# Kernel tuning notes

Measured on AMD Instinct MI355X. Metric: run time of the kernel, lower is better.

## Reference

```python
import jax, jax.numpy as jnp
import numpy as np
import math

B, S, DM = 32, 512, 1024   # batch (= groups*channels), seq_len, d_model
H, D, C = 16, 64, 8        # n_heads, d_kv, n_channels
NB, MD = 32, 128           # relative_attention_num_buckets, max_distance


def setup_inputs() -> dict:
    key = jax.random.key(0)
    ks = jax.random.split(key, 7)
    return {
        "hidden_states": jax.random.normal(ks[0], (B, S, DM), jnp.float32),
        "Wq": jax.random.normal(ks[1], (DM, H * D), jnp.float32) * 0.02,
        "Wk": jax.random.normal(ks[2], (DM, H * D), jnp.float32) * 0.02,
        "Wv": jax.random.normal(ks[3], (DM, H * D), jnp.float32) * 0.02,
        "Wo": jax.random.normal(ks[4], (H * D, DM), jnp.float32) * 0.02,
        "rel_emb": jax.random.normal(ks[5], (NB, H), jnp.float32) * 0.02,
        "beta": jax.random.normal(ks[6], (1, 1, H, 1, 1), jnp.float32) * 0.01,
    }


def _rel_bucket(relative_position, num_buckets=NB, max_distance=MD):
    # bidirectional (encoder) bucketing, faithful to T5
    nb = num_buckets // 2
    buckets = (relative_position > 0).astype(jnp.int32) * nb
    rp = jnp.abs(relative_position)
    max_exact = nb // 2
    is_small = rp < max_exact
    rp_safe = jnp.maximum(rp, 1).astype(jnp.float32)
    large = max_exact + (
        jnp.log(rp_safe / max_exact) / math.log(max_distance / max_exact) * (nb - max_exact)
    ).astype(jnp.int32)
    large = jnp.minimum(large, nb - 1)
    return buckets + jnp.where(is_small, rp, large)


def reference(hidden_states, Wq, Wk, Wv, Wo, rel_emb, beta):
    G = B // C  # groups

    def proj(W):
        # (B,S,DM) -> (B,S,H,D) -> (B,H,S,D) -> (G,C,H,S,D)
        x = (hidden_states @ W).reshape(B, S, H, D).transpose(0, 2, 1, 3)
        return x.reshape(G, C, H, S, D)

    q, k, v = proj(Wq), proj(Wk), proj(Wv)

    # relative position bias: (1,1,H,S,S)
    rel_pos = jnp.arange(S)[None, :] - jnp.arange(S)[:, None]
    bias = rel_emb[_rel_bucket(rel_pos)].transpose(2, 0, 1)[None, None]

    # local (dot-product) attention, T5-style: no 1/sqrt(d) scaling
    scores = jnp.einsum('gchsd,gchtd->gchst', q, k) + bias
    attn_w = jax.nn.softmax(scores, axis=-1)
    a_dot = jnp.einsum('gchst,gchtd->gchsd', attn_w, v)

    # compressive memory: ELU+1 feature map, summed over channels
    sk = jax.nn.elu(k) + 1.0
    M = jnp.einsum('gchsd,gchse->ghde', sk, v)   # (G,H,D,D)
    z = sk.sum(axis=3).sum(axis=1)               # (G,H,D)
    sq = jax.nn.elu(q) + 1.0
    num = jnp.einsum('gchsd,ghde->gchse', sq, M)
    den = jnp.einsum('gchsd,ghd->gchs', sq, z)[..., None] + 1e-6
    a_mem = num / den

    gate = jax.nn.sigmoid(beta)  # (1,1,H,1,1)
    out = gate * a_mem + (1.0 - gate) * a_dot

    # (G,C,H,S,D) -> (B,H,S,D) -> (B,S,H*D)
    out = out.reshape(B, H, S, D).transpose(0, 2, 1, 3).reshape(B, S, H * D)
    return out @ Wo
```

## Files before the change

kernel.cpp:

```cpp
#include <hip/hip_runtime.h>
#include <stdint.h>

typedef unsigned short u16;
typedef u16 u16x8 __attribute__((ext_vector_type(8)));
typedef u16 u16x4 __attribute__((ext_vector_type(4)));
typedef __bf16 bf16x8 __attribute__((ext_vector_type(8)));
typedef float f32x4 __attribute__((ext_vector_type(4)));

#define DEV static __device__ __forceinline__

DEV u16 f2bf(float f) {
  union { float f; uint32_t u; } v; v.f = f;
  uint32_t r = v.u + 0x7FFFu + ((v.u >> 16) & 1u);
  return (u16)(r >> 16);
}
DEV float bf2f(u16 s) {
  union { uint32_t u; float f; } v; v.u = ((uint32_t)s) << 16;
  return v.f;
}
DEV float elu1(float x) { return x > 0.f ? x + 1.f : __expf(x); }
DEV u16x8 ld8u(const u16* p) { return *reinterpret_cast<const u16x8*>(p); }

DEV f32x4 mfma16(u16x8 a, u16x8 b, f32x4 c) {
  return __builtin_amdgcn_mfma_f32_16x16x32_bf16(
      __builtin_bit_cast(bf16x8, a), __builtin_bit_cast(bf16x8, b), c, 0, 0, 0);
}
DEV void async16(void* lds, const void* g) {
  __builtin_amdgcn_global_load_lds(
      (__attribute__((address_space(1))) void*)g,
      (__attribute__((address_space(3))) void*)lds, 16, 0, 0);
}

#define BARR __builtin_amdgcn_s_barrier()
#define LG0  asm volatile("s_waitcnt lgkmcnt(0)" ::: "memory")
#define VMC(N) asm volatile("s_waitcnt vmcnt(" #N ")" ::: "memory")


__global__ __launch_bounds__(256) void k_cvt(const float* __restrict__ in, u16* __restrict__ out) {
  int i = blockIdx.x * 256 + threadIdx.x;
  const float4* p = reinterpret_cast<const float4*>(in) + (size_t)i * 2;
  float4 a = p[0], b = p[1];
  u16x8 o;
  o[0] = f2bf(a.x); o[1] = f2bf(a.y); o[2] = f2bf(a.z); o[3] = f2bf(a.w);
  o[4] = f2bf(b.x); o[5] = f2bf(b.y); o[6] = f2bf(b.z); o[7] = f2bf(b.w);
  reinterpret_cast<u16x8*>(out)[i] = o;
}

__global__ __launch_bounds__(1024) void k_tr(const float* __restrict__ Wq, const float* __restrict__ Wk,
                                             const float* __restrict__ Wv, const float* __restrict__ Wo,
                                             u16* __restrict__ wt, u16* __restrict__ wot) {
  __shared__ float tb[32][33];
  int mat = blockIdx.x >> 10;
  int tile = blockIdx.x & 1023;
  int n0 = (tile >> 5) * 32;
  int k0 = (tile & 31) * 32;
  const float* W = (mat == 0) ? Wq : (mat == 1) ? Wk : (mat == 2) ? Wv : Wo;
  int tx = threadIdx.x & 31, ty = threadIdx.x >> 5;
  tb[ty][tx] = W[(size_t)(k0 + ty) * 1024 + n0 + tx];
  __syncthreads();
  u16 v = f2bf(tb[tx][ty]);
  if (mat < 3) wt[(size_t)(mat * 1024 + n0 + ty) * 1024 + k0 + tx] = v;
  else         wot[(size_t)(n0 + ty) * 1024 + k0 + tx] = v;
}

__global__ void k_bias(const float* __restrict__ rel, float* __restrict__ bias) {
  int off = blockIdx.x * 256 + threadIdx.x;
  if (off >= 1023) return;
  int rp = off - 511;
  int bck = rp > 0 ? 16 : 0;
  int arp = rp < 0 ? -rp : rp;
  int idx;
  if (arp < 8) idx = arp;
  else {
    float l = logf((float)arp * 0.125f) / logf(16.0f) * 8.0f;
    int lg = 8 + (int)l;
    idx = lg < 15 ? lg : 15;
  }
  bck += idx;
  for (int h = 0; h < 16; ++h) bias[h * 1023 + off] = rel[bck * 16 + h];
}


template <int EPI>
__global__ __launch_bounds__(512, 3) void k_g256(const u16* __restrict__ A, const u16* __restrict__ Bt,
                                                 u16* __restrict__ oq, u16* __restrict__ ok2,
                                                 u16* __restrict__ ovt, float* __restrict__ of) {
  __shared__ __align__(16) u16 lsA[2][128 * 32];
  __shared__ __align__(16) u16 lsB[2][256 * 32];
  const int t = threadIdx.x;
  const int lane = t & 63, w = t >> 6;
  const int wm = w >> 2, wn = w & 3;
  const int lr = lane & 15, lg = lane >> 4;

  const int bid = blockIdx.x;
  const int xcd = bid & 7, local = bid >> 3;
  const int s = local >> 4, w16 = local & 15;
  const int msq = s & 3, nsq = s >> 2;
  const int m0 = (xcd * 16 + msq * 4 + (w16 >> 2)) * 128;
  const int n0 = (nsq * 4 + (w16 & 3)) * 256;

  auto stage = [&](int kt, int slot) {
    const int k0 = kt * 32;
    {
      int c = t, S = c >> 3, q = (c & 7) ^ (S & 7);
      int row = 2 * S + (q >> 2), u = q & 3;
      async16(&lsA[slot][c * 8], A + (size_t)(m0 + row) * 1024 + k0 + u * 8);
    }
#pragma unroll
    for (int i = 0; i < 2; ++i) {
      int c = i * 512 + t, S = c >> 3, q = (c & 7) ^ (S & 7);
      int row = 2 * S + (q >> 2), u = q & 3;
      async16(&lsB[slot][c * 8], Bt + (size_t)(n0 + row) * 1024 + k0 + u * 8);
    }
  };
  auto rdoff = [&](int r_) -> int {
    return (r_ >> 1) * 64 + (((((r_ & 1) << 2) + lg) ^ ((r_ >> 1) & 7)) << 3);
  };

  f32x4 acc[4][4];
#pragma unroll
  for (int i = 0; i < 4; ++i)
#pragma unroll
    for (int j = 0; j < 4; ++j) acc[i][j] = (f32x4){0.f, 0.f, 0.f, 0.f};

  stage(0, 0);
  stage(1, 1);
  VMC(3);
  BARR;

  for (int kt = 0; kt < 32; ++kt) {
    const int slot = kt & 1;
    const u16* la = &lsA[slot][0];
    const u16* lb = &lsB[slot][0];

    u16x8 af[4], bf[4];
#pragma unroll
    for (int mi = 0; mi < 4; ++mi) af[mi] = ld8u(la + rdoff(wm * 64 + mi * 16 + lr));
#pragma unroll
    for (int ni = 0; ni < 4; ++ni) bf[ni] = ld8u(lb + rdoff(wn * 64 + ni * 16 + lr));
    LG0;
    BARR;
    if (kt + 2 < 32) stage(kt + 2, slot);

    __builtin_amdgcn_s_setprio(1);
#pragma unroll
    for (int mi = 0; mi < 4; ++mi)
#pragma unroll
      for (int ni = 0; ni < 4; ++ni)
        acc[mi][ni] = mfma16(af[mi], bf[ni], acc[mi][ni]);
    __builtin_amdgcn_s_setprio(0);

    if (kt + 2 < 32)      { VMC(3); }
    else if (kt == 30)    { VMC(0); }
    BARR;
  }

  if (EPI == 0) {
    const int which = n0 >> 10;
    const int nb = (n0 & 1023) + wn * 64;
#pragma unroll
    for (int mi = 0; mi < 4; ++mi)
#pragma unroll
      for (int r = 0; r < 4; ++r) {
        int m = m0 + wm * 64 + mi * 16 + lg * 4 + r;
        int b = m >> 9, s2 = m & 511;
#pragma unroll
        for (int ni = 0; ni < 4; ++ni) {
          int nc = nb + ni * 16 + lr;
          int h = nc >> 6, d = nc & 63;
          int bh = b * 16 + h;
          u16 v = f2bf(acc[mi][ni][r]);
          if (which == 0)      oq[(size_t)(bh * 512 + s2) * 64 + d] = v;
          else if (which == 1) ok2[(size_t)(bh * 512 + s2) * 64 + d] = v;
          else                 ovt[(size_t)(bh * 64 + d) * 512 + s2] = v;
        }
      }
  } else {
#pragma unroll
    for (int mi = 0; mi < 4; ++mi)
#pragma unroll
      for (int r = 0; r < 4; ++r) {
        int m = m0 + wm * 64 + mi * 16 + lg * 4 + r;
#pragma unroll
        for (int ni = 0; ni < 4; ++ni) {
          int n = n0 + wn * 64 + ni * 16 + lr;
          of[(size_t)m * 1024 + n] = acc[mi][ni][r];
        }
      }
  }
}


__global__ __launch_bounds__(256) void k_mem(const u16* __restrict__ K, const u16* __restrict__ Vt,
                                             float* __restrict__ Mp, float* __restrict__ zp) {
  __shared__ __align__(16) u16 skT[64 * 128];
  __shared__ __align__(16) u16 lV[64 * 128];
  __shared__ float mbuf[64][65];
  __shared__ float zsh[4][64];
  const int bid = blockIdx.x;
  const int g = bid >> 7, h = (bid >> 3) & 15, c = bid & 7;
  const int bh = (g * 8 + c) * 16 + h;
  const u16* kp = K + (size_t)bh * 512 * 64;
  const u16* vp = Vt + (size_t)bh * 64 * 512;
  const int t = threadIdx.x, lane = t & 63, w = t >> 6;
  const int lr = lane & 15, lg = lane >> 4;
  const int dmy = t & 63, sq = t >> 6;

  f32x4 acc[4][4];
#pragma unroll
  for (int i = 0; i < 4; ++i)
#pragma unroll
    for (int j = 0; j < 4; ++j) acc[i][j] = (f32x4){0.f, 0.f, 0.f, 0.f};
  float zacc = 0.f;

  for (int s0 = 0; s0 < 512; s0 += 128) {
#pragma unroll
    for (int i = 0; i < 4; ++i) {
      int c2 = i * 256 + t;
      int row = c2 >> 4, u = c2 & 15;
      async16(lV + c2 * 8, vp + (size_t)row * 512 + s0 + ((u ^ (row & 7)) << 3));
    }
#pragma unroll
    for (int r = 0; r < 4; ++r) {
      const int un = sq + r * 4;
      const int ss0 = un * 8;
      u16x8 vals;
#pragma unroll
      for (int j = 0; j < 8; ++j) {
        float x = elu1(bf2f(kp[(size_t)(s0 + ss0 + j) * 64 + dmy]));
        zacc += x;
        vals[j] = f2bf(x);
      }
      *reinterpret_cast<u16x8*>(skT + dmy * 128 + ((un ^ (dmy & 7)) << 3)) = vals;
    }
    VMC(0);
    __syncthreads();
    u16x8 af[4], bfv[4];
#pragma unroll
    for (int ds = 0; ds < 4; ++ds) {
      const int d = ds * 16 + lr;
      af[ds] = ld8u(skT + d * 128 + (((w * 4 + lg) ^ (d & 7)) << 3));
    }
#pragma unroll
    for (int es = 0; es < 4; ++es) {
      const int e = es * 16 + lr;
      bfv[es] = ld8u(lV + e * 128 + (((w * 4 + lg) ^ (e & 7)) << 3));
    }
#pragma unroll
    for (int ds = 0; ds < 4; ++ds)
#pragma unroll
      for (int es = 0; es < 4; ++es) acc[ds][es] = mfma16(af[ds], bfv[es], acc[ds][es]);
    __syncthreads();
  }

  zsh[sq][dmy] = zacc;
  for (int wv = 0; wv < 4; ++wv) {
    if (w == wv) {
#pragma unroll
      for (int ds = 0; ds < 4; ++ds)
#pragma unroll
        for (int es = 0; es < 4; ++es)
#pragma unroll
          for (int r = 0; r < 4; ++r) {
            int d = ds * 16 + lg * 4 + r, e = es * 16 + lr;
            if (wv == 0) mbuf[d][e] = acc[ds][es][r];
            else         mbuf[d][e] += acc[ds][es][r];
          }
    }
    __syncthreads();
  }
#pragma unroll
  for (int j = 0; j < 16; ++j) {
    int idx = j * 256 + t;
    Mp[(size_t)bid * 4096 + idx] = mbuf[idx >> 6][idx & 63];
  }
  if (t < 64) zp[(size_t)bid * 64 + t] = zsh[0][t] + zsh[1][t] + zsh[2][t] + zsh[3][t];
}

__global__ __launch_bounds__(256) void k_red(const float* __restrict__ Mp, const float* __restrict__ zp,
                                             u16* __restrict__ Mt, float* __restrict__ zv) {
  const int gh = blockIdx.x;
  const int t = threadIdx.x;
#pragma unroll
  for (int j = 0; j < 16; ++j) {
    int idx = j * 256 + t;
    int d = idx >> 6, e = idx & 63;
    float s = 0.f;
#pragma unroll
    for (int c = 0; c < 8; ++c) s += Mp[(size_t)(gh * 8 + c) * 4096 + idx];
    Mt[(size_t)gh * 4096 + e * 64 + d] = f2bf(s);
  }
  if (t < 64) {
    float s = 0.f;
#pragma unroll
    for (int c = 0; c < 8; ++c) s += zp[(size_t)(gh * 8 + c) * 64 + t];
    zv[gh * 64 + t] = s;
  }
}


__global__ __launch_bounds__(256, 4) void k_attn(const u16* __restrict__ Q, const u16* __restrict__ K,
                                                 const u16* __restrict__ Vt, const u16* __restrict__ Mt,
                                                 const float* __restrict__ zv, const float* __restrict__ bias,
                                                 const float* __restrict__ beta, u16* __restrict__ blend) {
  __shared__ __align__(16) u16 lK[64 * 64];
  __shared__ __align__(16) u16 lV[64 * 64];
  __shared__ __align__(16) u16 ps[4][32 * 64];
  __shared__ float lbias[1023];
  __shared__ float zs[64];
  __shared__ float rsl[4][32];
  __shared__ float dnl[4][32];

  const int bid = blockIdx.x;
  const int bh = bid >> 2, qg = bid & 3;
  const int b = bh >> 4, h = bh & 15, g = b >> 3;
  const int gh = g * 16 + h;
  const int t = threadIdx.x, lane = t & 63, w = t >> 6;
  const int lr = lane & 15, lg = lane >> 4;
  const int q0w = qg * 128 + w * 32;
  const u16* qp = Q + (size_t)bh * 512 * 64;
  const u16* kp = K + (size_t)bh * 512 * 64;
  const u16* vp = Vt + (size_t)bh * 64 * 512;
  const u16* mp = Mt + (size_t)gh * 4096;
  const float gate = 1.f / (1.f + __expf(-beta[h]));
  u16* psw = &ps[w][0];

  for (int i = t; i < 1023; i += 256) lbias[i] = bias[h * 1023 + i];
  if (t < 64) zs[t] = zv[gh * 64 + t];

  u16x8 qf[2][2];
#pragma unroll
  for (int qs = 0; qs < 2; ++qs)
#pragma unroll
    for (int dc = 0; dc < 2; ++dc)
      qf[qs][dc] = ld8u(qp + (size_t)(q0w + qs * 16 + lr) * 64 + dc * 32 + lg * 8);

#pragma unroll
  for (int i = 0; i < 2; ++i) {
    int c = w * 128 + i * 64 + lane;
    int kr = c >> 3, u = c & 7;
    async16(lK + c * 8, kp + (size_t)kr * 64 + ((u ^ (kr & 7)) << 3));
    async16(lV + c * 8, vp + (size_t)kr * 512 + ((u ^ (kr & 7)) << 3));
  }
  __syncthreads();

#pragma unroll
  for (int qs = 0; qs < 2; ++qs) {
    float sum = 0.f;
#pragma unroll
    for (int dc = 0; dc < 2; ++dc)
#pragma unroll
      for (int j = 0; j < 8; ++j)
        sum += elu1(bf2f(qf[qs][dc][j])) * zs[dc * 32 + lg * 8 + j];
    sum += __shfl_xor(sum, 16, 64);
    sum += __shfl_xor(sum, 32, 64);
    if (lane < 16) dnl[w][qs * 16 + lane] = sum + 1e-6f;
  }

  f32x4 acc[2][4];
#pragma unroll
  for (int qs = 0; qs < 2; ++qs)
#pragma unroll
    for (int es = 0; es < 4; ++es) acc[qs][es] = (f32x4){0.f, 0.f, 0.f, 0.f};
  float rs[2] = {0.f, 0.f};

  for (int kt = 0; kt < 8; ++kt) {
#pragma unroll
    for (int ks = 0; ks < 4; ++ks) {
      const int kr = ks * 16 + lr;
      u16x8 kf0 = ld8u(lK + kr * 64 + (((0 * 4 + lg) ^ (kr & 7)) << 3));
      u16x8 kf1 = ld8u(lK + kr * 64 + (((1 * 4 + lg) ^ (kr & 7)) << 3));
#pragma unroll
      for (int qs = 0; qs < 2; ++qs) {
        f32x4 s = mfma16(kf0, qf[qs][0], (f32x4){0.f, 0.f, 0.f, 0.f});
        s = mfma16(kf1, qf[qs][1], s);
        const int bbase = kt * 64 + ks * 16 + lg * 4 - (q0w + qs * 16 + lr) + 511;
        u16x4 pk;
        float lsum = 0.f;
#pragma unroll
        for (int r = 0; r < 4; ++r) {
          float p = __expf(s[r] + lbias[bbase + r]);
          lsum += p;
          pk[r] = f2bf(p);
        }
        rs[qs] += lsum;
        const int row = qs * 16 + lr;
        const int addr = row * 64 + (((ks * 2 + (lg >> 1)) ^ (row & 7)) << 3) + (lg & 1) * 4;
        *reinterpret_cast<u16x4*>(psw + addr) = pk;
      }
    }
#pragma unroll
    for (int kc = 0; kc < 2; ++kc) {
      u16x8 pf[2];
#pragma unroll
      for (int qs = 0; qs < 2; ++qs) {
        const int row = qs * 16 + lr;
        pf[qs] = ld8u(psw + row * 64 + (((kc * 4 + lg) ^ (row & 7)) << 3));
      }
#pragma unroll
      for (int es = 0; es < 4; ++es) {
        const int er = es * 16 + lr;
        u16x8 vf = ld8u(lV + er * 64 + (((kc * 4 + lg) ^ (er & 7)) << 3));
#pragma unroll
        for (int qs = 0; qs < 2; ++qs) acc[qs][es] = mfma16(pf[qs], vf, acc[qs][es]);
      }
    }
    __syncthreads();
    if (kt + 1 < 8) {
#pragma unroll
      for (int i = 0; i < 2; ++i) {
        int c = w * 128 + i * 64 + lane;
        int kr = c >> 3, u = c & 7;
        async16(lK + c * 8, kp + (size_t)((kt + 1) * 64 + kr) * 64 + ((u ^ (kr & 7)) << 3));
        async16(lV + c * 8, vp + (size_t)kr * 512 + (kt + 1) * 64 + ((u ^ (kr & 7)) << 3));
      }
    }
    __syncthreads();
  }

#pragma unroll
  for (int qs = 0; qs < 2; ++qs) {
    float v = rs[qs];
    v += __shfl_xor(v, 16, 64);
    v += __shfl_xor(v, 32, 64);
    if (lane < 16) rsl[w][qs * 16 + lane] = 1.f / v;
  }

  u16x8 sqf[2][2];
#pragma unroll
  for (int qs = 0; qs < 2; ++qs)
#pragma unroll
    for (int dc = 0; dc < 2; ++dc)
#pragma unroll
      for (int j = 0; j < 8; ++j) sqf[qs][dc][j] = f2bf(elu1(bf2f(qf[qs][dc][j])));
  f32x4 am[2][4];
#pragma unroll
  for (int qs = 0; qs < 2; ++qs)
#pragma unroll
    for (int es = 0; es < 4; ++es) am[qs][es] = (f32x4){0.f, 0.f, 0.f, 0.f};
#pragma unroll
  for (int es = 0; es < 4; ++es)
#pragma unroll
    for (int dc = 0; dc < 2; ++dc) {
      u16x8 mf = ld8u(mp + (es * 16 + lr) * 64 + dc * 32 + lg * 8);
#pragma unroll
      for (int qs = 0; qs < 2; ++qs) am[qs][es] = mfma16(sqf[qs][dc], mf, am[qs][es]);
    }

#pragma unroll
  for (int qs = 0; qs < 2; ++qs)
#pragma unroll
    for (int r = 0; r < 4; ++r) {
      const int rowl = qs * 16 + lg * 4 + r;
      const float rinv = rsl[w][rowl];
      const float den = dnl[w][rowl];
      const int q = q0w + rowl;
#pragma unroll
      for (int es = 0; es < 4; ++es) {
        float o = gate * (am[qs][es][r] / den) + (1.f - gate) * acc[qs][es][r] * rinv;
        blend[(size_t)(b * 512 + q) * 1024 + h * 64 + es * 16 + lr] = f2bf(o);
      }
    }
}


extern "C" void kernel_launch(void* const* d_in, const int* in_sizes, int n_in,
                              void* d_out, int out_size, void* d_ws, size_t ws_size,
                              hipStream_t stream) {
  (void)in_sizes; (void)n_in; (void)out_size; (void)ws_size;
  const float* hs   = (const float*)d_in[0];
  const float* Wq   = (const float*)d_in[1];
  const float* Wk   = (const float*)d_in[2];
  const float* Wv   = (const float*)d_in[3];
  const float* Wo   = (const float*)d_in[4];
  const float* rel  = (const float*)d_in[5];
  const float* beta = (const float*)d_in[6];
  float* out = (float*)d_out;

  char* ws = (char*)d_ws;
  size_t off = 0;
  auto alloc = [&](size_t bytes) -> char* {
    char* p = ws + off;
    off += (bytes + 255) & ~(size_t)255;
    return p;
  };
  u16* hsb    = (u16*)alloc(16384ull * 1024 * 2);
  u16* wt     = (u16*)alloc(3072ull * 1024 * 2);
  u16* wot    = (u16*)alloc(1024ull * 1024 * 2);
  u16* q      = (u16*)alloc(16384ull * 1024 * 2);
  u16* k      = (u16*)alloc(16384ull * 1024 * 2);
  u16* vt     = (u16*)alloc(16384ull * 1024 * 2);
  float* Mp   = (float*)alloc(512ull * 4096 * 4);
  float* zp   = (float*)alloc(512ull * 64 * 4);
  u16* Mt     = (u16*)alloc(64ull * 4096 * 2);
  float* zv   = (float*)alloc(64ull * 64 * 4);
  float* bias = (float*)alloc(16ull * 1023 * 4);
  u16* blend  = hsb;

  k_cvt<<<8192, 256, 0, stream>>>(hs, hsb);
  k_tr<<<4096, 1024, 0, stream>>>(Wq, Wk, Wv, Wo, wt, wot);
  k_bias<<<4, 256, 0, stream>>>(rel, bias);
  k_g256<0><<<1536, 512, 0, stream>>>(hsb, wt, q, k, vt, nullptr);
  k_mem<<<512, 256, 0, stream>>>(k, vt, Mp, zp);
  k_red<<<64, 256, 0, stream>>>(Mp, zp, Mt, zv);
  k_attn<<<2048, 256, 0, stream>>>(q, k, vt, Mt, zv, bias, beta, blend);
  k_g256<1><<<512, 512, 0, stream>>>(blend, wot, nullptr, nullptr, nullptr, out);
}
```

Before: 341.7 us.

## Double-buffer K/V tiles in attention kernel and trim bias LDS window

Switches the attention kernel's K/V shared-memory tiles to two buffers, so the async load of the next tile is issued before computing on the current one, and waits with a partial vmcnt instead of a full sync-load-sync sequence. The relative-bias table in LDS is narrowed to the 640-entry window this query group needs, which offsets part of the extra LDS. Launch bounds drop from 4 to 3 blocks per CU to fit the larger shared footprint, which may reduce occupancy.

After: 339.4 us. Within noise of the previous version (-0.7%).

```diff
diff --git a/kernel.cpp b/kernel.cpp
--- a/kernel.cpp
+++ b/kernel.cpp
@@ -299,14 +299,14 @@
 }
 
 
-__global__ __launch_bounds__(256, 4) void k_attn(const u16* __restrict__ Q, const u16* __restrict__ K,
+__global__ __launch_bounds__(256, 3) void k_attn(const u16* __restrict__ Q, const u16* __restrict__ K,
                                                  const u16* __restrict__ Vt, const u16* __restrict__ Mt,
                                                  const float* __restrict__ zv, const float* __restrict__ bias,
                                                  const float* __restrict__ beta, u16* __restrict__ blend) {
-  __shared__ __align__(16) u16 lK[64 * 64];
-  __shared__ __align__(16) u16 lV[64 * 64];
+  __shared__ __align__(16) u16 lK[2][64 * 64];
+  __shared__ __align__(16) u16 lV[2][64 * 64];
   __shared__ __align__(16) u16 ps[4][32 * 64];
-  __shared__ float lbias[1023];
+  __shared__ float lbias[640];
   __shared__ float zs[64];
   __shared__ float rsl[4][32];
   __shared__ float dnl[4][32];
@@ -325,8 +325,19 @@
   const float gate = 1.f / (1.f + __expf(-beta[h]));
   u16* psw = &ps[w][0];
 
-  for (int i = t; i < 1023; i += 256) lbias[i] = bias[h * 1023 + i];
+  auto stage = [&](int kt, int sl) {
+#pragma unroll
+    for (int i = 0; i < 2; ++i) {
+      int c = w * 128 + i * 64 + lane;
+      int kr = c >> 3, u = c & 7;
+      async16(&lK[sl][c * 8], kp + (size_t)(kt * 64 + kr) * 64 + ((u ^ (kr & 7)) << 3));
+      async16(&lV[sl][c * 8], vp + (size_t)kr * 512 + kt * 64 + ((u ^ (kr & 7)) << 3));
+    }
+  };
+
+  for (int i = t; i < 640; i += 256) lbias[i] = bias[h * 1023 + i + 384 - qg * 128];
   if (t < 64) zs[t] = zv[gh * 64 + t];
+  LG0; BARR;
 
   u16x8 qf[2][2];
 #pragma unroll
@@ -334,15 +345,6 @@
 #pragma unroll
     for (int dc = 0; dc < 2; ++dc)
       qf[qs][dc] = ld8u(qp + (size_t)(q0w + qs * 16 + lr) * 64 + dc * 32 + lg * 8);
-
-#pragma unroll
-  for (int i = 0; i < 2; ++i) {
-    int c = w * 128 + i * 64 + lane;
-    int kr = c >> 3, u = c & 7;
-    async16(lK + c * 8, kp + (size_t)kr * 64 + ((u ^ (kr & 7)) << 3));
-    async16(lV + c * 8, vp + (size_t)kr * 512 + ((u ^ (kr & 7)) << 3));
-  }
-  __syncthreads();
 
 #pragma unroll
   for (int qs = 0; qs < 2; ++qs) {
@@ -357,6 +359,8 @@
     if (lane < 16) dnl[w][qs * 16 + lane] = sum + 1e-6f;
   }
 
+  stage(0, 0);
+
   f32x4 acc[2][4];
 #pragma unroll
   for (int qs = 0; qs < 2; ++qs)
@@ -365,21 +369,26 @@
   float rs[2] = {0.f, 0.f};
 
   for (int kt = 0; kt < 8; ++kt) {
+    const int sl = kt & 1;
+    if (kt + 1 < 8) stage(kt + 1, sl ^ 1);
+    if (kt + 1 < 8) { VMC(4); } else { VMC(0); }
+    BARR;
+
 #pragma unroll
     for (int ks = 0; ks < 4; ++ks) {
       const int kr = ks * 16 + lr;
-      u16x8 kf0 = ld8u(lK + kr * 64 + (((0 * 4 + lg) ^ (kr & 7)) << 3));
-      u16x8 kf1 = ld8u(lK + kr * 64 + (((1 * 4 + lg) ^ (kr & 7)) << 3));
+      u16x8 kf0 = ld8u(&lK[sl][kr * 64 + (((0 * 4 + lg) ^ (kr & 7)) << 3)]);
+      u16x8 kf1 = ld8u(&lK[sl][kr * 64 + (((1 * 4 + lg) ^ (kr & 7)) << 3)]);
 #pragma unroll
       for (int qs = 0; qs < 2; ++qs) {
         f32x4 s = mfma16(kf0, qf[qs][0], (f32x4){0.f, 0.f, 0.f, 0.f});
         s = mfma16(kf1, qf[qs][1], s);
-        const int bbase = kt * 64 + ks * 16 + lg * 4 - (q0w + qs * 16 + lr) + 511;
+        const int bb = kt * 64 + ks * 16 + lg * 4 - (w * 32 + qs * 16 + lr) + 127;
         u16x4 pk;
         float lsum = 0.f;
 #pragma unroll
         for (int r = 0; r < 4; ++r) {
-          float p = __expf(s[r] + lbias[bbase + r]);
+          float p = __expf(s[r] + lbias[bb + r]);
           lsum += p;
           pk[r] = f2bf(p);
         }
@@ -400,22 +409,12 @@
 #pragma unroll
       for (int es = 0; es < 4; ++es) {
         const int er = es * 16 + lr;
-        u16x8 vf = ld8u(lV + er * 64 + (((kc * 4 + lg) ^ (er & 7)) << 3));
+        u16x8 vf = ld8u(&lV[sl][er * 64 + (((kc * 4 + lg) ^ (er & 7)) << 3)]);
 #pragma unroll
         for (int qs = 0; qs < 2; ++qs) acc[qs][es] = mfma16(pf[qs], vf, acc[qs][es]);
       }
     }
-    __syncthreads();
-    if (kt + 1 < 8) {
-#pragma unroll
-      for (int i = 0; i < 2; ++i) {
-        int c = w * 128 + i * 64 + lane;
-        int kr = c >> 3, u = c & 7;
-        async16(lK + c * 8, kp + (size_t)((kt + 1) * 64 + kr) * 64 + ((u ^ (kr & 7)) << 3));
-        async16(lV + c * 8, vp + (size_t)kr * 512 + (kt + 1) * 64 + ((u ^ (kr & 7)) << 3));
-      }
-    }
-    __syncthreads();
+    BARR;
   }
 
 #pragma unroll
```
